# Performance work log

Measured on AMD Instinct MI355X. Metric: run time of the kernel, lower is better.

## Reference

```python
import jax, jax.numpy as jnp
import numpy as np
from jax import lax

DATA_NUM, CNUM, AUG_NUM, LNUM = 64, 6, 4, 3
B, H, W = 16, 512, 512
T_SEL = 0  # fixed aug selection (torch draws np.random.randint at runtime)
EPS = 1e-8
DN = ('NCHW', 'OIHW', 'NCHW')


def setup_inputs() -> dict:
    key = jax.random.key(0)
    ks = jax.random.split(key, 8)
    GLA_img_aug = jax.random.uniform(ks[0], (B, 1, H, W), dtype=jnp.float32)
    lbl = jax.random.randint(ks[1], (B, H, W), 0, CNUM, dtype=jnp.int32)
    index = jax.random.randint(ks[2], (B,), 0, DATA_NUM, dtype=jnp.int32)
    # learned params: Bezier control params (5+2=7 slots, only 0..3 used) and per-(sample,class,aug,layer) tiny conv pairs
    param = jax.random.uniform(ks[3], (DATA_NUM, CNUM, AUG_NUM, LNUM, 7), dtype=jnp.float32)
    w1 = 0.1 * jax.random.normal(ks[4], (DATA_NUM, CNUM, AUG_NUM, LNUM, 4, 1, 3, 3), dtype=jnp.float32)
    b1 = 0.01 * jax.random.normal(ks[5], (DATA_NUM, CNUM, AUG_NUM, LNUM, 4), dtype=jnp.float32)
    w2 = 0.1 * jax.random.normal(ks[6], (DATA_NUM, CNUM, AUG_NUM, LNUM, 1, 4, 3, 3), dtype=jnp.float32)
    b2 = 0.01 * jax.random.normal(ks[7], (DATA_NUM, CNUM, AUG_NUM, LNUM, 1), dtype=jnp.float32)
    return {"GLA_img_aug": GLA_img_aug, "lbl": lbl, "index": index,
            "param": param, "w1": w1, "b1": b1, "w2": w2, "b2": b2}


def _conv_pair(x, w1, b1, w2, b2):
    # x: [1,H,W]; per-sample Conv2d(1,4,3,p=1) -> Conv2d(4,1,3,p=1)
    y = lax.conv_general_dilated(x[None], w1, (1, 1), 'SAME', dimension_numbers=DN) + b1[None, :, None, None]
    y = lax.conv_general_dilated(y, w2, (1, 1), 'SAME', dimension_numbers=DN) + b2[None, :, None, None]
    return y[0]

_conv_batch = jax.vmap(_conv_pair)  # batched over per-sample weights


def _ftransfer(xn, lbl, i, index, param, w1, b1, w2, b2):
    raw = xn                                   # [B,1,H,W]
    mask = (lbl[:, None, :, :] == i)           # [B,1,H,W]
    c = xn * mask
    pp = jax.nn.sigmoid(param[index, i, T_SEL])   # [B,L,7]  (p := sigmoid)
    W1, B1 = w1[index, i, T_SEL], b1[index, i, T_SEL]
    W2, B2 = w2[index, i, T_SEL], b2[index, i, T_SEL]
    for layer in range(LNUM):
        p1 = pp[:, layer, 0][:, None, None, None]
        p2 = pp[:, layer, 1][:, None, None, None]
        p1v = pp[:, layer, 2][:, None, None, None]
        p2v = pp[:, layer, 3][:, None, None, None]
        mix = jax.nn.sigmoid(_conv_batch(raw, W1[:, layer], B1[:, layer], W2[:, layer], B2[:, layer]))
        om = 1.0 - c
        ct = 3.0 * om**2 * c * p1 + 3.0 * om * c**2 * p2 + c**3          # p0=0,  p3=1
        cv = om**3 + 3.0 * om**2 * c * p1v + 3.0 * om * c**2 * p2v       # p0v=1, p3v=0
        c = jnp.clip(ct * mix + cv * (1.0 - mix), 0.0, 1.0)
    # write back only where label == i (equivalent to torch's flag-filtered scatter)
    return jnp.where(mask, c, raw)


def reference(GLA_img_aug, lbl, index, param, w1, b1, w2, b2):
    x = GLA_img_aug
    mn = jnp.min(x, axis=(1, 2, 3), keepdims=True)
    mx = jnp.max(x, axis=(1, 2, 3), keepdims=True)
    scale = mx - mn + EPS
    xn = (x - mn) / scale
    for i in range(CNUM):
        xn = _ftransfer(xn, lbl, i, index, param, w1, b1, w2, b2)
    return xn * scale + mn
```

## Files before the change

kernel.cpp:

```cpp
#include <hip/hip_runtime.h>
#include <stdint.h>

#define HW 512
#define IMG (HW*HW)
#define CNUM_ 6

#define TILE 64
#define HALO 12
#define ST 88
#define SSTR 89
#define NT 512
#define RCAP 256

typedef float f2 __attribute__((ext_vector_type(2)));

#define LTOT 3840

#define OFF_MN 512
#define OFF_SC 528
#define OFF_INV 544
#define RECBASE 1024
#define REC_F 96
#define VARBASE (RECBASE + 96*REC_F)
#define VAR_F 27

__global__ __launch_bounds__(256) void k_minmax(const float4* __restrict__ x, float* __restrict__ wsf){
    int blk = blockIdx.x;
    int base4 = blk * 4096;
    float vmin = 1e30f, vmax = -1e30f;
#pragma unroll
    for (int k = 0; k < 16; k++){
        float4 v = x[base4 + k*256 + threadIdx.x];
        vmin = fminf(vmin, fminf(fminf(v.x, v.y), fminf(v.z, v.w)));
        vmax = fmaxf(vmax, fmaxf(fmaxf(v.x, v.y), fmaxf(v.z, v.w)));
    }
    __shared__ float smn[4], smx[4];
#pragma unroll
    for (int off = 32; off > 0; off >>= 1){
        vmin = fminf(vmin, __shfl_down(vmin, off));
        vmax = fmaxf(vmax, __shfl_down(vmax, off));
    }
    int wv = threadIdx.x >> 6;
    if ((threadIdx.x & 63) == 0){ smn[wv] = vmin; smx[wv] = vmax; }
    __syncthreads();
    if (threadIdx.x == 0){
        wsf[2*blk]     = fminf(fminf(smn[0], smn[1]), fminf(smn[2], smn[3]));
        wsf[2*blk + 1] = fmaxf(fmaxf(smx[0], smx[1]), fmaxf(smx[2], smx[3]));
    }
}

__global__ __launch_bounds__(256) void k_prep(const int* __restrict__ index, const float* __restrict__ param,
                       const float* __restrict__ w1, const float* __restrict__ b1,
                       const float* __restrict__ w2, const float* __restrict__ b2,
                       float* __restrict__ wsf){
    __shared__ float w1s[108], w2s[108], b1s[12], b2s[3], prm[21];
    const int r = blockIdx.x, t = threadIdx.x;
    if (r == 0 && t < 16){
        float mn = 1e30f, mx = -1e30f;
        for (int c = 0; c < 16; c++){
            mn = fminf(mn, wsf[2*(t*16 + c)]);
            mx = fmaxf(mx, wsf[2*(t*16 + c) + 1]);
        }
        float sc = mx - mn + 1e-8f;
        wsf[OFF_MN + t] = mn; wsf[OFF_SC + t] = sc; wsf[OFF_INV + t] = 1.0f / sc;
    }
    const int b = r / 6, i = r % 6;
    const int lb0 = (index[b]*CNUM_ + i) * 12;
    if (t < 108){
        int l = t / 36, j = t % 36;
        w1s[t] = w1[(lb0 + l)*36 + j];
        w2s[t] = w2[(lb0 + l)*36 + j];
    }
    if (t < 12) b1s[t] = b1[(lb0 + t/4)*4 + (t%4)];
    if (t < 3)  b2s[t] = b2[lb0 + t];
    if (t < 21) prm[t] = param[(lb0 + t/7)*7 + (t%7)];
    __syncthreads();
    float* rec = wsf + RECBASE + r*REC_F;
    float* var = wsf + VARBASE + r*9*3*VAR_F;
    for (int u = t; u < 9*3*26; u += 256){
        int kind = u / 78, rem = u % 78, l = rem / 26, e = rem % 26;
        int rowk = kind / 3, colk = kind % 3;
        if (e < 25){
            int ty = e/5 - 2, tx = e%5 - 2;
            float we = 0.f;
            for (int d = 0; d < 9; d++){
                int dy = d/3 - 1, dx = d%3 - 1;
                if ((rowk==0 && dy<0)||(rowk==2 && dy>0)||(colk==0 && dx<0)||(colk==2 && dx>0)) continue;
                int ey = ty - dy, ex = tx - dx;
                if (ey < -1 || ey > 1 || ex < -1 || ex > 1) continue;
                for (int c = 0; c < 4; c++)
                    we += w2s[l*36 + c*9 + d] * w1s[l*36 + c*9 + (ey+1)*3 + (ex+1)];
            }
            var[(kind*3 + l)*VAR_F + e] = we;
            if (kind == 4) rec[l*25 + e] = we;
        } else {
            float be = b2s[l];
            for (int c = 0; c < 4; c++){
                float sw = 0.f;
                for (int d = 0; d < 9; d++){
                    int dy = d/3 - 1, dx = d%3 - 1;
                    if ((rowk==0 && dy<0)||(rowk==2 && dy>0)||(colk==0 && dx<0)||(colk==2 && dx>0)) continue;
                    sw += w2s[l*36 + c*9 + d];
                }
                be += b1s[l*4 + c] * sw;
            }
            var[(kind*3 + l)*VAR_F + 25] = be;
            if (kind == 4) rec[75 + l] = be;
        }
    }
    if (t < 18){
        int l = t / 6, q = t % 6;
        float p1  = __builtin_amdgcn_rcpf(1.f + __expf(-prm[l*7 + 0]));
        float p2  = __builtin_amdgcn_rcpf(1.f + __expf(-prm[l*7 + 1]));
        float p1v = __builtin_amdgcn_rcpf(1.f + __expf(-prm[l*7 + 2]));
        float p2v = __builtin_amdgcn_rcpf(1.f + __expf(-prm[l*7 + 3]));
        float v;
        switch (q){
            case 0: v = 3.f*p1; break;
            case 1: v = 3.f*p2 - 6.f*p1; break;
            case 2: v = 1.f + 3.f*p1 - 3.f*p2; break;
            case 3: v = 3.f*p1v - 3.f; break;
            case 4: v = 3.f - 6.f*p1v + 3.f*p2v; break;
            default: v = -1.f + 3.f*p1v - 3.f*p2v; break;
        }
        rec[78 + l*6 + q] = v;
    }
}

__device__ __forceinline__ float sig1(float z){
    return __builtin_amdgcn_rcpf(1.f + __expf(-z));
}

__device__ __forceinline__ float bez3(float c, float mix, const float* __restrict__ cf){
    float ct = c * (cf[0] + c * (cf[1] + c * cf[2]));
    float cv = 1.f + c * (cf[3] + c * (cf[4] + c * cf[5]));
    float r = cv + mix * (ct - cv);
    return __builtin_amdgcn_fmed3f(r, 0.f, 1.f);
}

__device__ __forceinline__ f2 splat(float v){ f2 r = {v, v}; return r; }

__device__ __forceinline__ f2 sig2(f2 z){
    f2 r;
    r.x = __builtin_amdgcn_rcpf(1.f + __expf(-z.x));
    r.y = __builtin_amdgcn_rcpf(1.f + __expf(-z.y));
    return r;
}

__device__ __forceinline__ f2 bez3p(f2 c, f2 mix, const float* __restrict__ cf){
    f2 ct = c * (splat(cf[0]) + c * (splat(cf[1]) + c * splat(cf[2])));
    f2 cv = splat(1.f) + c * (splat(cf[3]) + c * (splat(cf[4]) + c * splat(cf[5])));
    f2 r = cv + mix * (ct - cv);
    r.x = __builtin_amdgcn_fmed3f(r.x, 0.f, 1.f);
    r.y = __builtin_amdgcn_fmed3f(r.y, 0.f, 1.f);
    return r;
}

__device__ __forceinline__ void load_taps(const float* __restrict__ s, int pos, float* tp){
    const float* sp0 = s + pos - (2*SSTR + 2);
    const float* sp1 = s + pos + (SSTR - 2);
#pragma unroll
    for (int wy = 0; wy < 3; wy++)
#pragma unroll
    for (int wx = 0; wx < 5; wx++)
        tp[wy*5 + wx] = sp0[wy*SSTR + wx];
#pragma unroll
    for (int wy = 0; wy < 2; wy++)
#pragma unroll
    for (int wx = 0; wx < 5; wx++)
        tp[15 + wy*5 + wx] = sp1[wy*SSTR + wx];
}

__device__ __forceinline__ void conv_px(const float* __restrict__ s, int pos,
                                        const float* __restrict__ rec,
                                        float& z0, float& z1, float& z2, float& cc){
    float tp[25];
    load_taps(s, pos, tp);
    f2 a0 = {rec[75], 0.f};
    f2 a1 = {rec[76], 0.f};
    f2 a2 = {rec[77], 0.f};
#pragma unroll
    for (int e = 0; e < 24; e += 2){
        f2 tv = {tp[e], tp[e+1]};
        f2 w0 = {rec[e],      rec[e+1]};
        f2 w1 = {rec[25 + e], rec[26 + e]};
        f2 w2 = {rec[50 + e], rec[51 + e]};
        a0 += w0 * tv;
        a1 += w1 * tv;
        a2 += w2 * tv;
    }
    float t24 = tp[24];
    z0 = a0.x + a0.y + rec[24]*t24;
    z1 = a1.x + a1.y + rec[49]*t24;
    z2 = a2.x + a2.y + rec[74]*t24;
    cc = tp[12];
}

__device__ __forceinline__ unsigned short* gl_addr(float* out, int sbase, int Y0, int X0, int e){
    return (unsigned short*)(out + sbase + (Y0 + HALO + (e >> 7))*HW + X0 + HALO) + (e & 127);
}

__global__ __launch_bounds__(NT, 8) void k_main(
        const float* __restrict__ x, const int* __restrict__ lbl,
        float* __restrict__ out, const float* __restrict__ wsf){
    __shared__ float s[ST*SSTR];
    __shared__ unsigned short lst[LTOT];
    __shared__ unsigned rlst[RCAP];
    __shared__ int cnt[8];
    const int lin = ((blockIdx.z << 3) + blockIdx.y) * 8 + blockIdx.x;
    const int tile = ((lin & 7) << 7) + (lin >> 3);
    const int bz = tile >> 6, by = (tile >> 3) & 7, bx = tile & 7;
    const int b = bz;
    const int X0 = bx * TILE - HALO, Y0 = by * TILE - HALO;
    const float mn = wsf[OFF_MN + b], sc = wsf[OFF_SC + b], inv = wsf[OFF_INV + b];
    const float mninv = mn * inv;
    const int tid = threadIdx.x;
    const int lane = tid & 63;
    const int sbase = b * IMG;
    const bool edgeblk = (bx == 0) | (bx == 7) | (by == 0) | (by == 7);

    if (tid < 8) cnt[tid] = 0;
    __syncthreads();

    for (int it = 0; it < 16; it++){
        int k = it*NT + tid;
        bool inb = k < ST*ST;
        int ly = k / ST, lx = k % ST;
        int gy = Y0 + ly, gx = X0 + lx;
        bool valid = inb && (unsigned)gy < (unsigned)HW && (unsigned)gx < (unsigned)HW;
        float v = 0.f; int c = 255;
        if (valid){
            int off = sbase + gy*HW + gx;
            v = x[off]*inv - mninv;
            c = lbl[off];
        }
        if (inb) s[ly*SSTR + lx] = v;
        int margin = min(min(lx, ST-1-lx), min(ly, ST-1-ly));
        bool ring = valid && ((gx==0) | (gx==HW-1) | (gy==0) | (gy==HW-1));
        bool mainok = valid && !ring && c < CNUM_ && margin >= 2 + 2*c;
        int ce = mainok ? c : 7;
        unsigned short pos = (unsigned short)(ly*SSTR + lx);

        unsigned long long m0 = __ballot(ce & 1);
        unsigned long long m1 = __ballot(ce & 2);
        unsigned long long m2 = __ballot(ce & 4);
        int basev = 0;
        if (lane < 6){
            unsigned long long mc = ((lane & 1) ? m0 : ~m0)
                                  & ((lane & 2) ? m1 : ~m1)
                                  & ((lane & 4) ? m2 : ~m2);
            int pc = __popcll(mc);
            if (pc) basev = atomicAdd(&cnt[lane], pc);
        }
        int mybase = __shfl(basev, ce < 6 ? ce : 0);
        if (mainok){
            unsigned long long mself = ((ce & 1) ? m0 : ~m0)
                                     & ((ce & 2) ? m1 : ~m1)
                                     & ((ce & 4) ? m2 : ~m2);
            int p = mybase + __popcll(mself & ((1ull << lane) - 1ull));
            if (ce < 3){
                int capc = 1408 - (ce << 7);
                int offc = ce * (1472 - (ce << 6));
                if (p < capc) lst[offc + p] = pos;
            } else {
                int d = ce - 3;
                int capc = 1056 - 96*d;
                int offc = d * (1104 - 48*d);
                if (p < capc) *gl_addr(out, sbase, Y0, X0, offc + p) = pos;
            }
        }
        if (edgeblk){
            bool ringok = ring && c < CNUM_ && margin >= 2;
            unsigned long long rm = __ballot(ringok);
            if (rm){
                int base = 0;
                if (lane == 0) base = atomicAdd(&cnt[6], __popcll(rm));
                base = __shfl(base, 0);
                if (ringok){
                    int p = base + __popcll(rm & ((1ull << lane) - 1ull));
                    if (p < RCAP) rlst[p] = ((unsigned)c << 16) | pos;
                }
            }
        }
    }
    __syncthreads();
    const int rn = min(cnt[6], RCAP);

    unsigned short pf[9];
#pragma unroll
    for (int d = 0; d < 3; d++){
        int capc = 1056 - 96*d;
        int offc = d * (1104 - 48*d);
        int nB = min(cnt[3 + d], capc);
#pragma unroll
        for (int sl = 0; sl < 3; sl++){
            int j = tid + sl*NT;
            unsigned short pv = 0;
            if (j < nB) pv = *gl_addr(out, sbase, Y0, X0, offc + j);
            pf[d*3 + sl] = pv;
        }
    }

#pragma unroll
    for (int cls = 0; cls < CNUM_; cls++){
        const int capc = (cls < 3) ? (1408 - (cls << 7)) : (1056 - 96*(cls - 3));
        const float* rec = wsf + RECBASE + (b*CNUM_ + cls)*REC_F;
        const int n = min(cnt[cls], capc);
        const int j0 = tid, j1 = tid + NT, j2 = tid + 2*NT;
        const bool v0 = j0 < n, v1 = j1 < n, v2 = j2 < n;
        int p0 = 0, p1 = 0, p2 = 0;
        if (cls < 3){
            const unsigned short* lp = lst + cls * (1472 - (cls << 6));
            if (v0) p0 = lp[j0];
            if (v1) p1 = lp[j1];
            if (v2) p2 = lp[j2];
        } else {
            p0 = pf[(cls-3)*3 + 0];
            p1 = pf[(cls-3)*3 + 1];
            p2 = pf[(cls-3)*3 + 2];
        }
        float z00=0.f, z01=0.f, z02=0.f, cc0=0.f;
        float z10=0.f, z11=0.f, z12=0.f, cc1=0.f;
        float u0, u1, u2;
        if (v0) conv_px(s, p0, rec, z00, z01, z02, cc0);
        if (v1) conv_px(s, p1, rec, z10, z11, z12, cc1);
        if (v0 | v1){
            f2 cP = {cc0, cc1};
            cP = bez3p(cP, sig2((f2){z00, z10}), rec + 78);
            cP = bez3p(cP, sig2((f2){z01, z11}), rec + 84);
            cP = bez3p(cP, sig2((f2){z02, z12}), rec + 90);
            u0 = cP.x; u1 = cP.y;
        }
        if (v2){
            float za, zb, zc, cc;
            conv_px(s, p2, rec, za, zb, zc, cc);
            cc = bez3(cc, sig1(za), rec + 78);
            cc = bez3(cc, sig1(zb), rec + 84);
            u2 = bez3(cc, sig1(zc), rec + 90);
        }
        int hav = -1; float rupd = 0.f;
        if (edgeblk && tid < rn){
            unsigned e = rlst[tid];
            int rc = (int)(e >> 16), pos = (int)(e & 0xffff);
            int ly = pos / SSTR, lx = pos % SSTR;
            int margin = min(min(lx, ST-1-lx), min(ly, ST-1-ly));
            if (rc == cls && margin >= 2 + 2*cls){
                int gy = Y0 + ly, gx = X0 + lx;
                int rowk = (gy == 0) ? 0 : ((gy == HW-1) ? 2 : 1);
                int colk = (gx == 0) ? 0 : ((gx == HW-1) ? 2 : 1);
                const float* vb = wsf + VARBASE + ((b*CNUM_ + cls)*9 + rowk*3 + colk)*3*VAR_F;
                float tp[25];
                load_taps(s, pos, tp);
                float c = tp[12];
#pragma unroll
                for (int l = 0; l < 3; l++){
                    float z = vb[l*VAR_F + 25];
#pragma unroll
                    for (int e2 = 0; e2 < 25; e2++) z += vb[l*VAR_F + e2] * tp[e2];
                    c = bez3(c, sig1(z), rec + 78 + 6*l);
                }
                rupd = c; hav = pos;
            }
        }
        __syncthreads();
        if (v0) s[p0] = u0;
        if (v1) s[p1] = u1;
        if (v2) s[p2] = u2;
        if (hav >= 0) s[hav] = rupd;
        __syncthreads();
    }

    for (int j = tid; j < TILE*TILE; j += NT){
        int py = j >> 6, px = j & 63;
        int gy = Y0 + HALO + py, gx = X0 + HALO + px;
        out[sbase + gy*HW + gx] = s[(HALO + py)*SSTR + (HALO + px)] * sc + mn;
    }
}

extern "C" void kernel_launch(void* const* d_in, const int* in_sizes, int n_in,
                              void* d_out, int out_size, void* d_ws, size_t ws_size,
                              hipStream_t stream){
    const float* x     = (const float*)d_in[0];
    const int*   lbl   = (const int*)  d_in[1];
    const int*   index = (const int*)  d_in[2];
    const float* param = (const float*)d_in[3];
    const float* w1    = (const float*)d_in[4];
    const float* b1    = (const float*)d_in[5];
    const float* w2    = (const float*)d_in[6];
    const float* b2    = (const float*)d_in[7];
    float* out = (float*)d_out;
    float* wsf = (float*)d_ws;

    k_minmax<<<256, 256, 0, stream>>>((const float4*)x, wsf);
    k_prep<<<96, 256, 0, stream>>>(index, param, w1, b1, w2, b2, wsf);
    dim3 g(8, 8, 16);
    k_main<<<g, NT, 0, stream>>>(x, lbl, out, wsf);
}
```

Before: 170.7 us.

## Merge minmax into prep kernel, software-pipeline tile loads, reduce norm in main

Folds the min/max reduction kernel into the prep kernel as extra blocks, which removes one launch. The final per-image min/max reduction moves into k_main, where each block does a 16-lane shuffle reduce. The tile fill loop is rewritten to prefetch two iterations ahead with clamped addresses and incremental index arithmetic in place of divide/modulo. Tap loads are also marked volatile, likely to control register pressure or scheduling. The price is redundant reduction work in every main block and volatile LDS loads that may block compiler optimisation.

```diff
diff --git a/kernel.cpp b/kernel.cpp
--- a/kernel.cpp
+++ b/kernel.cpp
@@ -16,53 +16,42 @@
 
 #define LTOT 3840
 
-#define OFF_MN 512
-#define OFF_SC 528
-#define OFF_INV 544
 #define RECBASE 1024
 #define REC_F 96
 #define VARBASE (RECBASE + 96*REC_F)
 #define VAR_F 27
 
-__global__ __launch_bounds__(256) void k_minmax(const float4* __restrict__ x, float* __restrict__ wsf){
-    int blk = blockIdx.x;
-    int base4 = blk * 4096;
-    float vmin = 1e30f, vmax = -1e30f;
-#pragma unroll
-    for (int k = 0; k < 16; k++){
-        float4 v = x[base4 + k*256 + threadIdx.x];
-        vmin = fminf(vmin, fminf(fminf(v.x, v.y), fminf(v.z, v.w)));
-        vmax = fmaxf(vmax, fmaxf(fmaxf(v.x, v.y), fmaxf(v.z, v.w)));
-    }
-    __shared__ float smn[4], smx[4];
-#pragma unroll
-    for (int off = 32; off > 0; off >>= 1){
-        vmin = fminf(vmin, __shfl_down(vmin, off));
-        vmax = fmaxf(vmax, __shfl_down(vmax, off));
-    }
-    int wv = threadIdx.x >> 6;
-    if ((threadIdx.x & 63) == 0){ smn[wv] = vmin; smx[wv] = vmax; }
-    __syncthreads();
-    if (threadIdx.x == 0){
-        wsf[2*blk]     = fminf(fminf(smn[0], smn[1]), fminf(smn[2], smn[3]));
-        wsf[2*blk + 1] = fmaxf(fmaxf(smx[0], smx[1]), fmaxf(smx[2], smx[3]));
-    }
-}
-
-__global__ __launch_bounds__(256) void k_prep(const int* __restrict__ index, const float* __restrict__ param,
+__global__ __launch_bounds__(256) void k_prep(const float4* __restrict__ x4,
+                       const int* __restrict__ index, const float* __restrict__ param,
                        const float* __restrict__ w1, const float* __restrict__ b1,
                        const float* __restrict__ w2, const float* __restrict__ b2,
                        float* __restrict__ wsf){
     __shared__ float w1s[108], w2s[108], b1s[12], b2s[3], prm[21];
+    __shared__ float smn[4], smx[4];
     const int r = blockIdx.x, t = threadIdx.x;
-    if (r == 0 && t < 16){
-        float mn = 1e30f, mx = -1e30f;
-        for (int c = 0; c < 16; c++){
-            mn = fminf(mn, wsf[2*(t*16 + c)]);
-            mx = fmaxf(mx, wsf[2*(t*16 + c) + 1]);
-        }
-        float sc = mx - mn + 1e-8f;
-        wsf[OFF_MN + t] = mn; wsf[OFF_SC + t] = sc; wsf[OFF_INV + t] = 1.0f / sc;
+    if (r >= 96){
+        int blk = r - 96;
+        int base4 = blk * 4096;
+        float vmin = 1e30f, vmax = -1e30f;
+#pragma unroll
+        for (int k = 0; k < 16; k++){
+            float4 v = x4[base4 + k*256 + t];
+            vmin = fminf(vmin, fminf(fminf(v.x, v.y), fminf(v.z, v.w)));
+            vmax = fmaxf(vmax, fmaxf(fmaxf(v.x, v.y), fmaxf(v.z, v.w)));
+        }
+#pragma unroll
+        for (int off = 32; off > 0; off >>= 1){
+            vmin = fminf(vmin, __shfl_down(vmin, off));
+            vmax = fmaxf(vmax, __shfl_down(vmax, off));
+        }
+        int wv = t >> 6;
+        if ((t & 63) == 0){ smn[wv] = vmin; smx[wv] = vmax; }
+        __syncthreads();
+        if (t == 0){
+            wsf[2*blk]     = fminf(fminf(smn[0], smn[1]), fminf(smn[2], smn[3]));
+            wsf[2*blk + 1] = fmaxf(fmaxf(smx[0], smx[1]), fmaxf(smx[2], smx[3]));
+        }
+        return;
     }
     const int b = r / 6, i = r % 6;
     const int lb0 = (index[b]*CNUM_ + i) * 12;
@@ -157,8 +146,8 @@
 }
 
 __device__ __forceinline__ void load_taps(const float* __restrict__ s, int pos, float* tp){
-    const float* sp0 = s + pos - (2*SSTR + 2);
-    const float* sp1 = s + pos + (SSTR - 2);
+    const volatile float* sp0 = s + pos - (2*SSTR + 2);
+    const volatile float* sp1 = s + pos + (SSTR - 2);
 #pragma unroll
     for (int wy = 0; wy < 3; wy++)
 #pragma unroll
@@ -207,39 +196,70 @@
     __shared__ unsigned short lst[LTOT];
     __shared__ unsigned rlst[RCAP];
     __shared__ int cnt[8];
+    __shared__ float snorm[4];
     const int lin = ((blockIdx.z << 3) + blockIdx.y) * 8 + blockIdx.x;
     const int tile = ((lin & 7) << 7) + (lin >> 3);
     const int bz = tile >> 6, by = (tile >> 3) & 7, bx = tile & 7;
     const int b = bz;
     const int X0 = bx * TILE - HALO, Y0 = by * TILE - HALO;
-    const float mn = wsf[OFF_MN + b], sc = wsf[OFF_SC + b], inv = wsf[OFF_INV + b];
-    const float mninv = mn * inv;
     const int tid = threadIdx.x;
     const int lane = tid & 63;
     const int sbase = b * IMG;
     const bool edgeblk = (bx == 0) | (bx == 7) | (by == 0) | (by == 7);
 
     if (tid < 8) cnt[tid] = 0;
+    if (tid < 16){
+        float pmn = wsf[2*(b*16 + tid)];
+        float pmx = wsf[2*(b*16 + tid) + 1];
+#pragma unroll
+        for (int off = 8; off > 0; off >>= 1){
+            pmn = fminf(pmn, __shfl_down(pmn, off));
+            pmx = fmaxf(pmx, __shfl_down(pmx, off));
+        }
+        if (tid == 0){
+            float scv = pmx - pmn + 1e-8f;
+            snorm[0] = pmn; snorm[1] = scv; snorm[2] = 1.0f / scv;
+        }
+    }
     __syncthreads();
-
+    const float mn = snorm[0], sc = snorm[1], inv = snorm[2];
+    const float mninv = mn * inv;
+
+#define ADV(yy, xx) { int w_ = (xx) + (NT % ST); int f_ = (w_ >= ST); \
+                      (xx) = w_ - (f_ ? ST : 0); (yy) += (NT/ST) + f_; }
+#define LOADPX(yy, xx, vv, cc) { \
+        int cy_ = min(max(Y0 + (yy), 0), HW-1); \
+        int cx_ = min(max(X0 + (xx), 0), HW-1); \
+        int o_ = sbase + cy_*HW + cx_; \
+        vv = x[o_]; cc = lbl[o_]; }
+
+    int y0c = tid / ST, x0c = tid % ST;
+    int y1c = y0c, x1c = x0c; ADV(y1c, x1c);
+    int y2c = y1c, x2c = x1c; ADV(y2c, x2c);
+    float vA, vB, vC; int cA, cB, cC;
+    LOADPX(y0c, x0c, vA, cA);
+    LOADPX(y1c, x1c, vB, cB);
+    LOADPX(y2c, x2c, vC, cC);
+
+#pragma unroll
     for (int it = 0; it < 16; it++){
-        int k = it*NT + tid;
-        bool inb = k < ST*ST;
-        int ly = k / ST, lx = k % ST;
-        int gy = Y0 + ly, gx = X0 + lx;
-        bool valid = inb && (unsigned)gy < (unsigned)HW && (unsigned)gx < (unsigned)HW;
-        float v = 0.f; int c = 255;
-        if (valid){
-            int off = sbase + gy*HW + gx;
-            v = x[off]*inv - mninv;
-            c = lbl[off];
-        }
+        const int ly = y0c, lx = x0c;
+        const bool inb = (it < 15) || (tid < ST*ST - 15*NT);
+        const int gy = Y0 + ly, gx = X0 + lx;
+        const bool valid = inb && (unsigned)gy < (unsigned)HW && (unsigned)gx < (unsigned)HW;
+        const float v = valid ? (vA*inv - mninv) : 0.f;
+        const int c = valid ? cA : 255;
         if (inb) s[ly*SSTR + lx] = v;
         int margin = min(min(lx, ST-1-lx), min(ly, ST-1-ly));
         bool ring = valid && ((gx==0) | (gx==HW-1) | (gy==0) | (gy==HW-1));
         bool mainok = valid && !ring && c < CNUM_ && margin >= 2 + 2*c;
         int ce = mainok ? c : 7;
         unsigned short pos = (unsigned short)(ly*SSTR + lx);
+
+        y0c = y1c; x0c = x1c; y1c = y2c; x1c = x2c;
+        vA = vB; cA = cB; vB = vC; cB = cC;
+        ADV(y2c, x2c);
+        if (it <= 12) LOADPX(y2c, x2c, vC, cC);
 
         unsigned long long m0 = __ballot(ce & 1);
         unsigned long long m1 = __ballot(ce & 2);
@@ -283,6 +303,8 @@
             }
         }
     }
+#undef ADV
+#undef LOADPX
     __syncthreads();
     const int rn = min(cnt[6], RCAP);
 
@@ -391,8 +413,7 @@
     float* out = (float*)d_out;
     float* wsf = (float*)d_ws;
 
-    k_minmax<<<256, 256, 0, stream>>>((const float4*)x, wsf);
-    k_prep<<<96, 256, 0, stream>>>(index, param, w1, b1, w2, b2, wsf);
+    k_prep<<<352, 256, 0, stream>>>((const float4*)x, index, param, w1, b1, w2, b2, wsf);
     dim3 g(8, 8, 16);
     k_main<<<g, NT, 0, stream>>>(x, lbl, out, wsf);
 }
```

New measurement: 174.0 us. Within noise of the previous version (+1.9%).
